# Performance work log

Measured on AMD Instinct MI355X. Metric: run time of the kernel, lower is better.

## Reference

```python
import jax, jax.numpy as jnp
import numpy as np

B, S, D_IN, D_OUT = 4, 2048, 1024, 1024

def setup_inputs() -> dict:
    key = jax.random.key(0)
    k1, k2, k3, k4, k5, k6 = jax.random.split(key, 6)
    return {
        "inputs_for_keys": jax.random.normal(k1, (B, S, D_IN), dtype=jnp.float32),
        "inputs_for_values": jax.random.normal(k2, (B, S, D_IN), dtype=jnp.float32),
        "inputs_for_queries": jax.random.normal(k3, (B, S, D_IN), dtype=jnp.float32),
        "WK": jax.random.truncated_normal(k4, -2.0, 2.0, (D_IN, D_OUT), dtype=jnp.float32) * 0.1,
        "WV": jax.random.truncated_normal(k5, -2.0, 2.0, (D_IN, D_OUT), dtype=jnp.float32) * 0.1,
        "WQ": jax.random.truncated_normal(k6, -2.0, 2.0, (D_IN, D_OUT), dtype=jnp.float32) * 0.1,
    }

def reference(inputs_for_keys, inputs_for_values, inputs_for_queries, WK, WV, WQ):
    # projections: [B,S,D_in] @ [D_in,D_out] -> [B,S,D_out]
    K = jnp.einsum('bsd,de->bse', inputs_for_keys, WK)
    V = jnp.einsum('bsd,de->bse', inputs_for_values, WV)
    Q = jnp.einsum('bsd,de->bse', inputs_for_queries, WQ)
    # scores: [B,S,S]. NOTE: original TF code scales by sqrt(K.shape[1]) = sqrt(seq_len),
    # not sqrt(head_dim) — reproduce that faithfully.
    scale = jnp.sqrt(jnp.float32(K.shape[1]))
    scores = jnp.einsum('bqe,bke->bqk', Q, K) / scale
    attn = jax.nn.softmax(scores, axis=-1)
    return jnp.einsum('bqk,bke->bqe', attn, V)
```

## Files before the change

kernel.cpp:

```cpp
#include <hip/hip_runtime.h>
#include <hip/hip_bf16.h>


typedef __attribute__((ext_vector_type(4))) float    f32x4;
typedef __attribute__((ext_vector_type(8))) _Float16 f16x8;
typedef __attribute__((ext_vector_type(4))) _Float16 f16x4;

constexpr size_t MiB = 1u << 20;
constexpr size_t MK  = (size_t)8192 * 1024;
constexpr size_t WSZ = (size_t)1024 * 1024;

__device__ __forceinline__ void gload_lds16(const void* g, void* l) {
  __builtin_amdgcn_global_load_lds(
      (const __attribute__((address_space(1))) unsigned int*)g,
      (__attribute__((address_space(3))) unsigned int*)l, 16, 0, 0);
}

#define MFMA16(a, b, c) __builtin_amdgcn_mfma_f32_16x16x32_f16(a, b, c, 0, 0, 0)

__device__ __forceinline__ void swz_block(int& bx, int& by, int& bz) {
  unsigned gx = gridDim.x, gy = gridDim.y;
  unsigned flat = blockIdx.x + gx * (blockIdx.y + gy * blockIdx.z);
  unsigned total = gx * gy * gridDim.z;
  unsigned cpx = total >> 3;
  unsigned s = (flat & 7) * cpx + (flat >> 3);
  bx = s % gx; s /= gx; by = s % gy; bz = s / gy;
}

__global__ __launch_bounds__(256) void convert_x(
    const float* __restrict__ x0, const float* __restrict__ x1,
    const float* __restrict__ x2, _Float16* __restrict__ XF)
{
  const int z = blockIdx.z;
  const float* x = z == 0 ? x0 : (z == 1 ? x1 : x2);
  size_t i = ((size_t)blockIdx.x * 256 + threadIdx.x) * 4;
  float4 v = *(const float4*)(x + i);
  f16x4 h = {(_Float16)v.x, (_Float16)v.y, (_Float16)v.z, (_Float16)v.w};
  *(f16x4*)(XF + (size_t)z * MK + i) = h;
}

__global__ __launch_bounds__(256) void transpose_conv_w(
    const float* __restrict__ w0, const float* __restrict__ w1,
    const float* __restrict__ w2, _Float16* __restrict__ WT)
{
  const int z = blockIdx.z;
  const float* W = z == 0 ? w0 : (z == 1 ? w1 : w2);
  _Float16* o = WT + (size_t)z * WSZ;
  __shared__ float tile[32][33];
  const int bx = blockIdx.x * 32;
  const int by = blockIdx.y * 32;
  const int tx = threadIdx.x & 31, ty = threadIdx.x >> 5;
  #pragma unroll
  for (int r = 0; r < 32; r += 8)
    tile[ty + r][tx] = W[(size_t)(by + ty + r) * 1024 + bx + tx];
  __syncthreads();
  #pragma unroll
  for (int r = 0; r < 32; r += 8)
    o[(size_t)(bx + ty + r) * 1024 + by + tx] = (_Float16)tile[tx][ty + r];
}

__global__ __launch_bounds__(256) void transpose_v(
    const _Float16* __restrict__ V, _Float16* __restrict__ Vt)
{
  const _Float16* v = V + (size_t)blockIdx.z * 2048 * 1024;
  _Float16* o = Vt + (size_t)blockIdx.z * 1024 * 2048;
  __shared__ _Float16 tile[32][33];
  const int bx = blockIdx.x * 32;
  const int by = blockIdx.y * 32;
  const int tx = threadIdx.x & 31, ty = threadIdx.x >> 5;
  #pragma unroll
  for (int r = 0; r < 32; r += 8)
    tile[ty + r][tx] = v[(size_t)(by + ty + r) * 1024 + bx + tx];
  __syncthreads();
  #pragma unroll
  for (int r = 0; r < 32; r += 8)
    o[(size_t)(bx + ty + r) * 2048 + by + tx] = tile[tx][ty + r];
}

template <int MODE>
__global__ __launch_bounds__(512, 2) void gemm256(
    const _Float16* __restrict__ At, size_t sA,
    const _Float16* __restrict__ Bt, size_t sB,
    void* __restrict__ C0v, size_t sCz,
    int N, int K, float scale)
{
  extern __shared__ char lds[];
  constexpr int BB = 128 * 64;
  char* ldsAb = lds;
  char* ldsBb = lds + 65536;

  int bx, by, bz;
  swz_block(bx, by, bz);
  const _Float16* A = At + (size_t)bz * sA;
  const _Float16* B = Bt + (size_t)bz * sB;

  const int gm0 = by * 256;
  const int gn0 = bx * 128;
  const int tid = threadIdx.x;
  const int lane = tid & 63, wave = tid >> 6;
  const int wm = (wave >> 1) * 64;
  const int wn = (wave & 1) * 64;
  const int fr = lane & 15, fq = lane >> 4;

  const int nkt = K >> 5;

  const int cbs = (((tid & 3) ^ ((tid >> 3) & 3)) << 4);
  const size_t aOff = (size_t)(gm0 + (tid >> 2)) * K + (cbs >> 1);
  const size_t bOff = (size_t)(gn0 + (tid >> 2)) * K + (cbs >> 1);
  const int cbr  = (fq * 16) ^ (((fr >> 1) & 3) << 4);
  const int arow = (wm + fr) * 64 + cbr;
  const int brow = (wn + fr) * 64 + cbr;

  f32x4 acc[4][4] = {};

  for (int tp = 0; tp < 3; ++tp) {
    const _Float16* gA = A + aOff + tp * 32;
    const _Float16* gB = B + bOff + tp * 32;
    char* dA = ldsAb + tp * 16384 + tid * 16;
    char* dB = ldsBb + tp * BB + tid * 16;
    gload_lds16(gA, dA);
    gload_lds16(gA + (size_t)128 * K, dA + 8192);
    gload_lds16(gB, dB);
  }
  asm volatile("s_waitcnt vmcnt(6)" ::: "memory");
  __builtin_amdgcn_s_barrier();
  __builtin_amdgcn_sched_barrier(0);

  for (int t = 0; t < nkt; ++t) {
    const char* pA = ldsAb + (t & 3) * 16384;
    const char* pB = ldsBb + (t & 3) * BB;
    const int tp = t + 3;
    const bool st = tp < nkt;
    const _Float16* gA = A + aOff + (st ? tp : 0) * 32;
    const _Float16* gB = B + bOff + (st ? tp : 0) * 32;
    char* dA = ldsAb + (tp & 3) * 16384 + tid * 16;
    char* dB = ldsBb + (tp & 3) * BB + tid * 16;

    if (st) { gload_lds16(gA, dA); gload_lds16(gB, dB); }
    f16x8 bfr[4], af[2];
    #pragma unroll
    for (int n = 0; n < 4; ++n) bfr[n] = *(const f16x8*)(pB + brow + n * 1024);
    #pragma unroll
    for (int m = 0; m < 2; ++m) af[m] = *(const f16x8*)(pA + arow + m * 1024);
    __builtin_amdgcn_s_setprio(1);
    #pragma unroll
    for (int m = 0; m < 2; ++m)
      #pragma unroll
      for (int n = 0; n < 4; ++n) acc[m][n] = MFMA16(af[m], bfr[n], acc[m][n]);
    __builtin_amdgcn_s_setprio(0);
    __builtin_amdgcn_s_barrier();
    __builtin_amdgcn_sched_barrier(0);

    if (st) gload_lds16(gA + (size_t)128 * K, dA + 8192);
    #pragma unroll
    for (int m = 0; m < 2; ++m) af[m] = *(const f16x8*)(pA + arow + (m + 2) * 1024);
    __builtin_amdgcn_s_setprio(1);
    #pragma unroll
    for (int m = 0; m < 2; ++m)
      #pragma unroll
      for (int n = 0; n < 4; ++n) acc[m + 2][n] = MFMA16(af[m], bfr[n], acc[m + 2][n]);
    __builtin_amdgcn_s_setprio(0);
    asm volatile("s_waitcnt vmcnt(6)" ::: "memory");
    __builtin_amdgcn_s_barrier();
    __builtin_amdgcn_sched_barrier(0);
  }

  const int erow = gm0 + wm + fq * 4;
  const int ecol = gn0 + wn + fr;
  if constexpr (MODE == 0) {
    float* C = (float*)C0v + (size_t)bz * sCz;
    #pragma unroll
    for (int m = 0; m < 4; ++m)
      #pragma unroll
      for (int n = 0; n < 4; ++n) {
        size_t base = (size_t)(erow + m * 16) * N + (ecol + n * 16);
        #pragma unroll
        for (int r = 0; r < 4; ++r)
          C[base + (size_t)r * N] = acc[m][n][r] * scale;
      }
  } else {
    _Float16* C = (_Float16*)C0v + (size_t)bz * sCz;
    #pragma unroll
    for (int m = 0; m < 4; ++m)
      #pragma unroll
      for (int n = 0; n < 4; ++n) {
        size_t base = (size_t)(erow + m * 16) * N + (ecol + n * 16);
        #pragma unroll
        for (int r = 0; r < 4; ++r)
          C[base + (size_t)r * N] = (_Float16)acc[m][n][r];
      }
  }
}

__global__ __launch_bounds__(256) void softmax_rows(
    const float* __restrict__ S, _Float16* __restrict__ P)
{
  const size_t row = blockIdx.x;
  const float4* srow = (const float4*)(S + row * 2048);
  const int t = threadIdx.x;
  float4 v0 = srow[t];
  float4 v1 = srow[t + 256];

  float m = fmaxf(fmaxf(fmaxf(v0.x, v0.y), fmaxf(v0.z, v0.w)),
                  fmaxf(fmaxf(v1.x, v1.y), fmaxf(v1.z, v1.w)));
  #pragma unroll
  for (int o = 32; o >= 1; o >>= 1) m = fmaxf(m, __shfl_xor(m, o));
  __shared__ float redm[4];
  if ((t & 63) == 0) redm[t >> 6] = m;
  __syncthreads();
  m = fmaxf(fmaxf(redm[0], redm[1]), fmaxf(redm[2], redm[3]));

  float e[8];
  e[0] = __expf(v0.x - m); e[1] = __expf(v0.y - m);
  e[2] = __expf(v0.z - m); e[3] = __expf(v0.w - m);
  e[4] = __expf(v1.x - m); e[5] = __expf(v1.y - m);
  e[6] = __expf(v1.z - m); e[7] = __expf(v1.w - m);
  float s = e[0] + e[1] + e[2] + e[3] + e[4] + e[5] + e[6] + e[7];
  #pragma unroll
  for (int o = 32; o >= 1; o >>= 1) s += __shfl_xor(s, o);
  __shared__ float reds[4];
  if ((t & 63) == 0) reds[t >> 6] = s;
  __syncthreads();
  s = reds[0] + reds[1] + reds[2] + reds[3];

  const float inv = 1.0f / s;
  f16x4 p0 = {(_Float16)(e[0] * inv), (_Float16)(e[1] * inv),
              (_Float16)(e[2] * inv), (_Float16)(e[3] * inv)};
  f16x4 p1 = {(_Float16)(e[4] * inv), (_Float16)(e[5] * inv),
              (_Float16)(e[6] * inv), (_Float16)(e[7] * inv)};
  f16x4* prow = (f16x4*)(P + row * 2048);
  prow[t] = p0;
  prow[t + 256] = p1;
}

extern "C" void kernel_launch(void* const* d_in, const int* in_sizes, int n_in,
                              void* d_out, int out_size, void* d_ws, size_t ws_size,
                              hipStream_t stream)
{
  const float* Xk = (const float*)d_in[0];
  const float* Xv = (const float*)d_in[1];
  const float* Xq = (const float*)d_in[2];
  const float* WK = (const float*)d_in[3];
  const float* WV = (const float*)d_in[4];
  const float* WQ = (const float*)d_in[5];
  float* out = (float*)d_out;
  char* ws = (char*)d_ws;

  _Float16* XF  = (_Float16*)(ws);
  _Float16* WT  = (_Float16*)(ws + 48 * MiB);
  _Float16* PROJ= (_Float16*)(ws + 54 * MiB);
  _Float16* VT  = (_Float16*)(ws + 102 * MiB);
  float*   SCORES = (float*)(ws + 118 * MiB);
  _Float16* P   = (_Float16*)(ws);

  _Float16* Kp = PROJ;
  _Float16* Vp = PROJ + MK;
  _Float16* Qp = PROJ + 2 * MK;

  auto* fP  = gemm256<1>;
  auto* fSC = gemm256<0>;
  (void)hipFuncSetAttribute((const void*)fP,  hipFuncAttributeMaxDynamicSharedMemorySize, 98304);
  (void)hipFuncSetAttribute((const void*)fSC, hipFuncAttributeMaxDynamicSharedMemorySize, 98304);

  convert_x<<<dim3(8192, 1, 3), 256, 0, stream>>>(Xk, Xv, Xq, XF);
  transpose_conv_w<<<dim3(32, 32, 3), 256, 0, stream>>>(WK, WV, WQ, WT);
  gemm256<1><<<dim3(8, 32, 3), 512, 98304, stream>>>(
      XF, MK, WT, WSZ, PROJ, MK, 1024, 1024, 1.0f);
  transpose_v<<<dim3(32, 64, 4), 256, 0, stream>>>(Vp, VT);
  gemm256<0><<<dim3(16, 8, 4), 512, 98304, stream>>>(
      Qp, (size_t)2048 * 1024, Kp, (size_t)2048 * 1024,
      SCORES, (size_t)2048 * 2048, 2048, 1024, 0.022097086912079608f);
  softmax_rows<<<dim3(8192), 256, 0, stream>>>(SCORES, P);
  gemm256<0><<<dim3(8, 8, 4), 512, 98304, stream>>>(
      P, (size_t)2048 * 2048, VT, (size_t)1024 * 2048,
      out, (size_t)2048 * 1024, 1024, 2048, 1.0f);
}
```

Measured before the change: 222.1 us.

## Add 256x256 eight-phase GEMM and store fp16 scores with wave-per-row softmax

Adds a new gemm8p kernel with 256x256 output tiles, 128 KiB double-buffered LDS and a four-phase interleaved load/MFMA schedule. It is used for the projection and QK^T GEMMs to raise data reuse per tile. The score matrix is now written in fp16 instead of fp32, which halves score traffic, and softmax is rewritten to one wave per row with no LDS reductions. Storing scaled scores in fp16 loses some precision, and the larger tiles mean fewer blocks, which lowers occupancy and load balance.

New measurement: 202.4 us. 1.1x faster.

```diff
diff --git a/kernel.cpp b/kernel.cpp
--- a/kernel.cpp
+++ b/kernel.cpp
@@ -75,6 +75,167 @@
   #pragma unroll
   for (int r = 0; r < 32; r += 8)
     o[(size_t)(bx + ty + r) * 2048 + by + tx] = tile[tx][ty + r];
+}
+
+template <int MODE>
+__global__ __launch_bounds__(512, 2) void gemm8p(
+    const _Float16* __restrict__ At, size_t sA,
+    const _Float16* __restrict__ Bt, size_t sB,
+    void* __restrict__ Cv, size_t sCz,
+    int N, int K, float scale)
+{
+  extern __shared__ char lds[];
+  int bx, by, bz;
+  swz_block(bx, by, bz);
+  const _Float16* A = At + (size_t)bz * sA;
+  const _Float16* B = Bt + (size_t)bz * sB;
+
+  const int gm0 = by * 256, gn0 = bx * 256;
+  const int tid = threadIdx.x;
+  const int lane = tid & 63, wave = tid >> 6;
+  const int wm = (wave >> 2) * 128;
+  const int wn = (wave & 3) * 64;
+  const int fr = lane & 15, fq = lane >> 4;
+  const int nkt = K >> 6;
+
+  const int clog = ((tid & 7) ^ ((tid >> 3) & 7)) * 8;
+  const _Float16* srcA = A + (size_t)(gm0 + (tid >> 3)) * K + clog;
+  const _Float16* srcB = B + (size_t)(gn0 + (tid >> 3)) * K + clog;
+  char* const dst0 = lds + tid * 16;
+
+  auto SH = [&](int tile, int h) {
+    const _Float16* s = (h < 2 ? srcA : srcB) + (size_t)((h & 1) * 128) * K
+                        + tile * 64;
+    char* d = dst0 + (tile & 1) * 65536 + h * 16384;
+    gload_lds16(s, d);
+    gload_lds16(s + (size_t)64 * K, d + 8192);
+  };
+
+  const int axor = fr & 7;
+  const int pc0 = (fq ^ axor) * 16;
+  const int pc1 = ((4 + fq) ^ axor) * 16;
+  const int arb = (wm + fr) * 128;
+  const int brb = 32768 + (wn + fr) * 128;
+
+  f32x4 acc[8][4] = {};
+  f16x8 af[4][2], b0[2][2], b1[2][2];
+
+  SH(0, 0); SH(0, 1); SH(0, 2); SH(0, 3);
+  if (nkt > 1) {
+    SH(1, 0);
+    asm volatile("s_waitcnt vmcnt(2)" ::: "memory");
+  } else {
+    asm volatile("s_waitcnt vmcnt(0)" ::: "memory");
+  }
+  __builtin_amdgcn_s_barrier();
+  __builtin_amdgcn_sched_barrier(0);
+
+#define PHASE_MID                                          \
+  __builtin_amdgcn_s_barrier();                            \
+  asm volatile("s_waitcnt lgkmcnt(0)" ::: "memory");       \
+  __builtin_amdgcn_sched_barrier(0);                       \
+  __builtin_amdgcn_s_setprio(1);
+#define PHASE_END                                          \
+  __builtin_amdgcn_s_setprio(0);                           \
+  __builtin_amdgcn_sched_barrier(0);                       \
+  __builtin_amdgcn_s_barrier();
+
+  for (int t = 0; t < nkt; ++t) {
+    const char* buf = lds + (t & 1) * 65536;
+    const bool st1 = (t + 1) < nkt;
+
+    #pragma unroll
+    for (int mi = 0; mi < 4; ++mi) {
+      af[mi][0] = *(const f16x8*)(buf + arb + mi * 2048 + pc0);
+      af[mi][1] = *(const f16x8*)(buf + arb + mi * 2048 + pc1);
+    }
+    #pragma unroll
+    for (int ni = 0; ni < 2; ++ni) {
+      b0[ni][0] = *(const f16x8*)(buf + brb + ni * 2048 + pc0);
+      b0[ni][1] = *(const f16x8*)(buf + brb + ni * 2048 + pc1);
+    }
+    if (st1) SH(t + 1, 1);
+    PHASE_MID
+    #pragma unroll
+    for (int mi = 0; mi < 4; ++mi)
+      #pragma unroll
+      for (int ni = 0; ni < 2; ++ni)
+        #pragma unroll
+        for (int kk = 0; kk < 2; ++kk)
+          acc[mi][ni] = MFMA16(af[mi][kk], b0[ni][kk], acc[mi][ni]);
+    PHASE_END
+
+    #pragma unroll
+    for (int ni = 0; ni < 2; ++ni) {
+      b1[ni][0] = *(const f16x8*)(buf + brb + (ni + 2) * 2048 + pc0);
+      b1[ni][1] = *(const f16x8*)(buf + brb + (ni + 2) * 2048 + pc1);
+    }
+    if (st1) SH(t + 1, 2);
+    PHASE_MID
+    #pragma unroll
+    for (int mi = 0; mi < 4; ++mi)
+      #pragma unroll
+      for (int ni = 0; ni < 2; ++ni)
+        #pragma unroll
+        for (int kk = 0; kk < 2; ++kk)
+          acc[mi][ni + 2] = MFMA16(af[mi][kk], b1[ni][kk], acc[mi][ni + 2]);
+    PHASE_END
+
+    #pragma unroll
+    for (int mi = 0; mi < 4; ++mi) {
+      af[mi][0] = *(const f16x8*)(buf + arb + (mi + 4) * 2048 + pc0);
+      af[mi][1] = *(const f16x8*)(buf + arb + (mi + 4) * 2048 + pc1);
+    }
+    if (st1) SH(t + 1, 3);
+    PHASE_MID
+    #pragma unroll
+    for (int mi = 0; mi < 4; ++mi)
+      #pragma unroll
+      for (int ni = 0; ni < 2; ++ni)
+        #pragma unroll
+        for (int kk = 0; kk < 2; ++kk)
+          acc[mi + 4][ni] = MFMA16(af[mi][kk], b0[ni][kk], acc[mi + 4][ni]);
+    PHASE_END
+
+    const bool st2 = (t + 2) < nkt;
+    if (st2) SH(t + 2, 0);
+    __builtin_amdgcn_s_barrier();
+    __builtin_amdgcn_s_setprio(1);
+    #pragma unroll
+    for (int mi = 0; mi < 4; ++mi)
+      #pragma unroll
+      for (int ni = 0; ni < 2; ++ni)
+        #pragma unroll
+        for (int kk = 0; kk < 2; ++kk)
+          acc[mi + 4][ni + 2] = MFMA16(af[mi][kk], b1[ni][kk], acc[mi + 4][ni + 2]);
+    __builtin_amdgcn_s_setprio(0);
+    __builtin_amdgcn_sched_barrier(0);
+    if (st2) asm volatile("s_waitcnt vmcnt(2)" ::: "memory");
+    else     asm volatile("s_waitcnt vmcnt(0)" ::: "memory");
+    __builtin_amdgcn_s_barrier();
+  }
+#undef PHASE_MID
+#undef PHASE_END
+
+  const int erow = gm0 + wm + fq * 4;
+  const int ecol = gn0 + wn + fr;
+  #pragma unroll
+  for (int m = 0; m < 8; ++m)
+    #pragma unroll
+    for (int n = 0; n < 4; ++n) {
+      size_t base = (size_t)(erow + m * 16) * N + (ecol + n * 16);
+      #pragma unroll
+      for (int r = 0; r < 4; ++r) {
+        float v = acc[m][n][r];
+        if constexpr (MODE == 0)
+          ((float*)Cv + (size_t)bz * sCz)[base + (size_t)r * N] = v * scale;
+        else if constexpr (MODE == 1)
+          ((_Float16*)Cv + (size_t)bz * sCz)[base + (size_t)r * N] = (_Float16)v;
+        else
+          ((_Float16*)Cv + (size_t)bz * sCz)[base + (size_t)r * N] =
+              (_Float16)(v * scale);
+      }
+    }
 }
 
 template <int MODE>
@@ -167,70 +328,59 @@
 
   const int erow = gm0 + wm + fq * 4;
   const int ecol = gn0 + wn + fr;
-  if constexpr (MODE == 0) {
-    float* C = (float*)C0v + (size_t)bz * sCz;
-    #pragma unroll
-    for (int m = 0; m < 4; ++m)
-      #pragma unroll
-      for (int n = 0; n < 4; ++n) {
-        size_t base = (size_t)(erow + m * 16) * N + (ecol + n * 16);
-        #pragma unroll
-        for (int r = 0; r < 4; ++r)
-          C[base + (size_t)r * N] = acc[m][n][r] * scale;
-      }
-  } else {
-    _Float16* C = (_Float16*)C0v + (size_t)bz * sCz;
-    #pragma unroll
-    for (int m = 0; m < 4; ++m)
-      #pragma unroll
-      for (int n = 0; n < 4; ++n) {
-        size_t base = (size_t)(erow + m * 16) * N + (ecol + n * 16);
-        #pragma unroll
-        for (int r = 0; r < 4; ++r)
-          C[base + (size_t)r * N] = (_Float16)acc[m][n][r];
-      }
+  float* C = (float*)C0v + (size_t)bz * sCz;
+  #pragma unroll
+  for (int m = 0; m < 4; ++m)
+    #pragma unroll
+    for (int n = 0; n < 4; ++n) {
+      size_t base = (size_t)(erow + m * 16) * N + (ecol + n * 16);
+      #pragma unroll
+      for (int r = 0; r < 4; ++r)
+        C[base + (size_t)r * N] = acc[m][n][r] * scale;
+    }
+}
+
+__global__ __launch_bounds__(256) void softmax_rows(
+    const _Float16* __restrict__ S, _Float16* __restrict__ P)
+{
+  const int w = threadIdx.x >> 6, lane = threadIdx.x & 63;
+  const size_t row = (size_t)blockIdx.x * 4 + w;
+  const _Float16* sr = S + row * 2048;
+
+  f16x8 v[4];
+  #pragma unroll
+  for (int c = 0; c < 4; ++c)
+    v[c] = *(const f16x8*)(sr + c * 512 + lane * 8);
+
+  float m = -1e30f;
+  #pragma unroll
+  for (int c = 0; c < 4; ++c)
+    #pragma unroll
+    for (int j = 0; j < 8; ++j) m = fmaxf(m, (float)v[c][j]);
+  #pragma unroll
+  for (int o = 32; o >= 1; o >>= 1) m = fmaxf(m, __shfl_xor(m, o));
+
+  float e[4][8];
+  float s = 0.f;
+  #pragma unroll
+  for (int c = 0; c < 4; ++c)
+    #pragma unroll
+    for (int j = 0; j < 8; ++j) {
+      e[c][j] = __expf((float)v[c][j] - m);
+      s += e[c][j];
+    }
+  #pragma unroll
+  for (int o = 32; o >= 1; o >>= 1) s += __shfl_xor(s, o);
+
+  const float inv = 1.0f / s;
+  _Float16* pr = P + row * 2048;
+  #pragma unroll
+  for (int c = 0; c < 4; ++c) {
+    f16x8 p;
+    #pragma unroll
+    for (int j = 0; j < 8; ++j) p[j] = (_Float16)(e[c][j] * inv);
+    *(f16x8*)(pr + c * 512 + lane * 8) = p;
   }
-}
-
-__global__ __launch_bounds__(256) void softmax_rows(
-    const float* __restrict__ S, _Float16* __restrict__ P)
-{
-  const size_t row = blockIdx.x;
-  const float4* srow = (const float4*)(S + row * 2048);
-  const int t = threadIdx.x;
-  float4 v0 = srow[t];
-  float4 v1 = srow[t + 256];
-
-  float m = fmaxf(fmaxf(fmaxf(v0.x, v0.y), fmaxf(v0.z, v0.w)),
-                  fmaxf(fmaxf(v1.x, v1.y), fmaxf(v1.z, v1.w)));
-  #pragma unroll
-  for (int o = 32; o >= 1; o >>= 1) m = fmaxf(m, __shfl_xor(m, o));
-  __shared__ float redm[4];
-  if ((t & 63) == 0) redm[t >> 6] = m;
-  __syncthreads();
-  m = fmaxf(fmaxf(redm[0], redm[1]), fmaxf(redm[2], redm[3]));
-
-  float e[8];
-  e[0] = __expf(v0.x - m); e[1] = __expf(v0.y - m);
-  e[2] = __expf(v0.z - m); e[3] = __expf(v0.w - m);
-  e[4] = __expf(v1.x - m); e[5] = __expf(v1.y - m);
-  e[6] = __expf(v1.z - m); e[7] = __expf(v1.w - m);
-  float s = e[0] + e[1] + e[2] + e[3] + e[4] + e[5] + e[6] + e[7];
-  #pragma unroll
-  for (int o = 32; o >= 1; o >>= 1) s += __shfl_xor(s, o);
-  __shared__ float reds[4];
-  if ((t & 63) == 0) reds[t >> 6] = s;
-  __syncthreads();
-  s = reds[0] + reds[1] + reds[2] + reds[3];
-
-  const float inv = 1.0f / s;
-  f16x4 p0 = {(_Float16)(e[0] * inv), (_Float16)(e[1] * inv),
-              (_Float16)(e[2] * inv), (_Float16)(e[3] * inv)};
-  f16x4 p1 = {(_Float16)(e[4] * inv), (_Float16)(e[5] * inv),
-              (_Float16)(e[6] * inv), (_Float16)(e[7] * inv)};
-  f16x4* prow = (f16x4*)(P + row * 2048);
-  prow[t] = p0;
-  prow[t + 256] = p1;
 }
 
 extern "C" void kernel_launch(void* const* d_in, const int* in_sizes, int n_in,
@@ -246,31 +396,33 @@
   float* out = (float*)d_out;
   char* ws = (char*)d_ws;
 
-  _Float16* XF  = (_Float16*)(ws);
-  _Float16* WT  = (_Float16*)(ws + 48 * MiB);
-  _Float16* PROJ= (_Float16*)(ws + 54 * MiB);
-  _Float16* VT  = (_Float16*)(ws + 102 * MiB);
-  float*   SCORES = (float*)(ws + 118 * MiB);
-  _Float16* P   = (_Float16*)(ws);
+  _Float16* XF   = (_Float16*)(ws);
+  _Float16* WT   = (_Float16*)(ws + 48 * MiB);
+  _Float16* PROJ = (_Float16*)(ws + 54 * MiB);
+  _Float16* VT   = (_Float16*)(ws + 102 * MiB);
+  _Float16* SC   = (_Float16*)(ws + 118 * MiB);
+  _Float16* P    = (_Float16*)(ws);
 
   _Float16* Kp = PROJ;
   _Float16* Vp = PROJ + MK;
   _Float16* Qp = PROJ + 2 * MK;
 
-  auto* fP  = gemm256<1>;
-  auto* fSC = gemm256<0>;
-  (void)hipFuncSetAttribute((const void*)fP,  hipFuncAttributeMaxDynamicSharedMemorySize, 98304);
-  (void)hipFuncSetAttribute((const void*)fSC, hipFuncAttributeMaxDynamicSharedMemorySize, 98304);
+  auto* fP  = gemm8p<1>;
+  auto* fSC = gemm8p<2>;
+  auto* fPV = gemm256<0>;
+  (void)hipFuncSetAttribute((const void*)fP,  hipFuncAttributeMaxDynamicSharedMemorySize, 131072);
+  (void)hipFuncSetAttribute((const void*)fSC, hipFuncAttributeMaxDynamicSharedMemorySize, 131072);
+  (void)hipFuncSetAttribute((const void*)fPV, hipFuncAttributeMaxDynamicSharedMemorySize, 98304);
 
   convert_x<<<dim3(8192, 1, 3), 256, 0, stream>>>(Xk, Xv, Xq, XF);
   transpose_conv_w<<<dim3(32, 32, 3), 256, 0, stream>>>(WK, WV, WQ, WT);
-  gemm256<1><<<dim3(8, 32, 3), 512, 98304, stream>>>(
+  gemm8p<1><<<dim3(4, 32, 3), 512, 131072, stream>>>(
       XF, MK, WT, WSZ, PROJ, MK, 1024, 1024, 1.0f);
   transpose_v<<<dim3(32, 64, 4), 256, 0, stream>>>(Vp, VT);
-  gemm256<0><<<dim3(16, 8, 4), 512, 98304, stream>>>(
+  gemm8p<2><<<dim3(8, 8, 4), 512, 131072, stream>>>(
       Qp, (size_t)2048 * 1024, Kp, (size_t)2048 * 1024,
-      SCORES, (size_t)2048 * 2048, 2048, 1024, 0.022097086912079608f);
-  softmax_rows<<<dim3(8192), 256, 0, stream>>>(SCORES, P);
+      SC, (size_t)2048 * 2048, 2048, 1024, 0.022097086912079608f);
+  softmax_rows<<<dim3(2048), 256, 0, stream>>>(SC, P);
   gemm256<0><<<dim3(8, 8, 4), 512, 98304, stream>>>(
       P, (size_t)2048 * 2048, VT, (size_t)1024 * 2048,
       out, (size_t)2048 * 1024, 1024, 2048, 1.0f);
```

## Rework GEMM pipeline to 3-stage buffers, store scores in fp16, wave-per-row softmax

Applied to the files above, without the earlier changes.

The GEMM kernel drops from a 4-deep split-phase LDS pipeline (96KB) to a 3-deep single-phase pipeline (72KB) with one barrier per k-tile, a new swizzle pattern and a higher occupancy hint in launch bounds. The attention scores are now written in fp16 rather than fp32, which halves score write and read traffic. Softmax processes one row per wave using shuffle reductions only, with no LDS reductions or block syncs. The fp16 scores lose some precision before the softmax, and the shallower prefetch may hide less memory latency.

Measured after the change: 208.1 us. 1.07x faster.

```diff
diff --git a/kernel.cpp b/kernel.cpp
--- a/kernel.cpp
+++ b/kernel.cpp
@@ -78,159 +78,145 @@
 }
 
 template <int MODE>
-__global__ __launch_bounds__(512, 2) void gemm256(
+__global__ __launch_bounds__(512, 4) void gemmO(
     const _Float16* __restrict__ At, size_t sA,
     const _Float16* __restrict__ Bt, size_t sB,
-    void* __restrict__ C0v, size_t sCz,
+    void* __restrict__ Cv, size_t sCz,
     int N, int K, float scale)
 {
   extern __shared__ char lds[];
-  constexpr int BB = 128 * 64;
-  char* ldsAb = lds;
-  char* ldsBb = lds + 65536;
-
   int bx, by, bz;
   swz_block(bx, by, bz);
   const _Float16* A = At + (size_t)bz * sA;
   const _Float16* B = Bt + (size_t)bz * sB;
 
-  const int gm0 = by * 256;
-  const int gn0 = bx * 128;
+  const int gm0 = by * 256, gn0 = bx * 128;
   const int tid = threadIdx.x;
   const int lane = tid & 63, wave = tid >> 6;
   const int wm = (wave >> 1) * 64;
   const int wn = (wave & 1) * 64;
   const int fr = lane & 15, fq = lane >> 4;
-
   const int nkt = K >> 5;
 
-  const int cbs = (((tid & 3) ^ ((tid >> 3) & 3)) << 4);
-  const size_t aOff = (size_t)(gm0 + (tid >> 2)) * K + (cbs >> 1);
-  const size_t bOff = (size_t)(gn0 + (tid >> 2)) * K + (cbs >> 1);
-  const int cbr  = (fq * 16) ^ (((fr >> 1) & 3) << 4);
-  const int arow = (wm + fr) * 64 + cbr;
-  const int brow = (wn + fr) * 64 + cbr;
+  const int clog = ((tid & 3) ^ ((tid >> 2) & 3)) * 8;
+  const _Float16* srcA = A + (size_t)(gm0 + (tid >> 2)) * K + clog;
+  const _Float16* srcB = B + (size_t)(gn0 + (tid >> 2)) * K + clog;
+  char* const dst0 = lds + tid * 16;
+
+  auto STG = [&](int tile) {
+    const int off = tile * 32;
+    char* d = dst0 + (tile % 3) * 24576;
+    gload_lds16(srcA + off,                  d);
+    gload_lds16(srcA + off + (size_t)128 * K, d + 8192);
+    gload_lds16(srcB + off,                  d + 16384);
+  };
+
+  const int pc  = (fq ^ (fr & 3)) * 16;
+  const int arb = (wm + fr) * 64 + pc;
+  const int brb = 16384 + (wn + fr) * 64 + pc;
 
   f32x4 acc[4][4] = {};
-
-  for (int tp = 0; tp < 3; ++tp) {
-    const _Float16* gA = A + aOff + tp * 32;
-    const _Float16* gB = B + bOff + tp * 32;
-    char* dA = ldsAb + tp * 16384 + tid * 16;
-    char* dB = ldsBb + tp * BB + tid * 16;
-    gload_lds16(gA, dA);
-    gload_lds16(gA + (size_t)128 * K, dA + 8192);
-    gload_lds16(gB, dB);
+  f16x8 af[4], bfr[4];
+
+  STG(0);
+  if (nkt > 1) {
+    STG(1);
+    asm volatile("s_waitcnt vmcnt(3)" ::: "memory");
+  } else {
+    asm volatile("s_waitcnt vmcnt(0)" ::: "memory");
   }
-  asm volatile("s_waitcnt vmcnt(6)" ::: "memory");
   __builtin_amdgcn_s_barrier();
   __builtin_amdgcn_sched_barrier(0);
 
   for (int t = 0; t < nkt; ++t) {
-    const char* pA = ldsAb + (t & 3) * 16384;
-    const char* pB = ldsBb + (t & 3) * BB;
-    const int tp = t + 3;
-    const bool st = tp < nkt;
-    const _Float16* gA = A + aOff + (st ? tp : 0) * 32;
-    const _Float16* gB = B + bOff + (st ? tp : 0) * 32;
-    char* dA = ldsAb + (tp & 3) * 16384 + tid * 16;
-    char* dB = ldsBb + (tp & 3) * BB + tid * 16;
-
-    if (st) { gload_lds16(gA, dA); gload_lds16(gB, dB); }
-    f16x8 bfr[4], af[2];
-    #pragma unroll
-    for (int n = 0; n < 4; ++n) bfr[n] = *(const f16x8*)(pB + brow + n * 1024);
-    #pragma unroll
-    for (int m = 0; m < 2; ++m) af[m] = *(const f16x8*)(pA + arow + m * 1024);
+    const char* buf = lds + (t % 3) * 24576;
+    const bool st2 = (t + 2) < nkt;
+
+    if (st2) STG(t + 2);
+
+    #pragma unroll
+    for (int mi = 0; mi < 4; ++mi)
+      af[mi] = *(const f16x8*)(buf + arb + mi * 1024);
+    #pragma unroll
+    for (int ni = 0; ni < 4; ++ni)
+      bfr[ni] = *(const f16x8*)(buf + brb + ni * 1024);
+
     __builtin_amdgcn_s_setprio(1);
     #pragma unroll
-    for (int m = 0; m < 2; ++m)
+    for (int mi = 0; mi < 4; ++mi)
       #pragma unroll
-      for (int n = 0; n < 4; ++n) acc[m][n] = MFMA16(af[m], bfr[n], acc[m][n]);
+      for (int ni = 0; ni < 4; ++ni)
+        acc[mi][ni] = MFMA16(af[mi], bfr[ni], acc[mi][ni]);
     __builtin_amdgcn_s_setprio(0);
-    __builtin_amdgcn_s_barrier();
-    __builtin_amdgcn_sched_barrier(0);
-
-    if (st) gload_lds16(gA + (size_t)128 * K, dA + 8192);
-    #pragma unroll
-    for (int m = 0; m < 2; ++m) af[m] = *(const f16x8*)(pA + arow + (m + 2) * 1024);
-    __builtin_amdgcn_s_setprio(1);
-    #pragma unroll
-    for (int m = 0; m < 2; ++m)
-      #pragma unroll
-      for (int n = 0; n < 4; ++n) acc[m + 2][n] = MFMA16(af[m], bfr[n], acc[m + 2][n]);
-    __builtin_amdgcn_s_setprio(0);
-    asm volatile("s_waitcnt vmcnt(6)" ::: "memory");
+
+    if (st2)               asm volatile("s_waitcnt vmcnt(3)" ::: "memory");
+    else if (t + 1 < nkt)  asm volatile("s_waitcnt vmcnt(0)" ::: "memory");
     __builtin_amdgcn_s_barrier();
     __builtin_amdgcn_sched_barrier(0);
   }
 
   const int erow = gm0 + wm + fq * 4;
   const int ecol = gn0 + wn + fr;
-  if constexpr (MODE == 0) {
-    float* C = (float*)C0v + (size_t)bz * sCz;
-    #pragma unroll
-    for (int m = 0; m < 4; ++m)
+  #pragma unroll
+  for (int m = 0; m < 4; ++m)
+    #pragma unroll
+    for (int n = 0; n < 4; ++n) {
+      size_t base = (size_t)(erow + m * 16) * N + (ecol + n * 16);
       #pragma unroll
-      for (int n = 0; n < 4; ++n) {
-        size_t base = (size_t)(erow + m * 16) * N + (ecol + n * 16);
-        #pragma unroll
-        for (int r = 0; r < 4; ++r)
-          C[base + (size_t)r * N] = acc[m][n][r] * scale;
+      for (int r = 0; r < 4; ++r) {
+        float v = acc[m][n][r];
+        if constexpr (MODE == 0)
+          ((float*)Cv + (size_t)bz * sCz)[base + (size_t)r * N] = v * scale;
+        else if constexpr (MODE == 1)
+          ((_Float16*)Cv + (size_t)bz * sCz)[base + (size_t)r * N] = (_Float16)v;
+        else
+          ((_Float16*)Cv + (size_t)bz * sCz)[base + (size_t)r * N] =
+              (_Float16)(v * scale);
       }
-  } else {
-    _Float16* C = (_Float16*)C0v + (size_t)bz * sCz;
-    #pragma unroll
-    for (int m = 0; m < 4; ++m)
-      #pragma unroll
-      for (int n = 0; n < 4; ++n) {
-        size_t base = (size_t)(erow + m * 16) * N + (ecol + n * 16);
-        #pragma unroll
-        for (int r = 0; r < 4; ++r)
-          C[base + (size_t)r * N] = (_Float16)acc[m][n][r];
-      }
+    }
+}
+
+__global__ __launch_bounds__(256) void softmax_rows(
+    const _Float16* __restrict__ S, _Float16* __restrict__ P)
+{
+  const int w = threadIdx.x >> 6, lane = threadIdx.x & 63;
+  const size_t row = (size_t)blockIdx.x * 4 + w;
+  const _Float16* sr = S + row * 2048;
+
+  f16x8 v[4];
+  #pragma unroll
+  for (int c = 0; c < 4; ++c)
+    v[c] = *(const f16x8*)(sr + c * 512 + lane * 8);
+
+  float m = -1e30f;
+  #pragma unroll
+  for (int c = 0; c < 4; ++c)
+    #pragma unroll
+    for (int j = 0; j < 8; ++j) m = fmaxf(m, (float)v[c][j]);
+  #pragma unroll
+  for (int o = 32; o >= 1; o >>= 1) m = fmaxf(m, __shfl_xor(m, o));
+
+  float e[4][8];
+  float s = 0.f;
+  #pragma unroll
+  for (int c = 0; c < 4; ++c)
+    #pragma unroll
+    for (int j = 0; j < 8; ++j) {
+      e[c][j] = __expf((float)v[c][j] - m);
+      s += e[c][j];
+    }
+  #pragma unroll
+  for (int o = 32; o >= 1; o >>= 1) s += __shfl_xor(s, o);
+
+  const float inv = 1.0f / s;
+  _Float16* pr = P + row * 2048;
+  #pragma unroll
+  for (int c = 0; c < 4; ++c) {
+    f16x8 p;
+    #pragma unroll
+    for (int j = 0; j < 8; ++j) p[j] = (_Float16)(e[c][j] * inv);
+    *(f16x8*)(pr + c * 512 + lane * 8) = p;
   }
-}
-
-__global__ __launch_bounds__(256) void softmax_rows(
-    const float* __restrict__ S, _Float16* __restrict__ P)
-{
-  const size_t row = blockIdx.x;
-  const float4* srow = (const float4*)(S + row * 2048);
-  const int t = threadIdx.x;
-  float4 v0 = srow[t];
-  float4 v1 = srow[t + 256];
-
-  float m = fmaxf(fmaxf(fmaxf(v0.x, v0.y), fmaxf(v0.z, v0.w)),
-                  fmaxf(fmaxf(v1.x, v1.y), fmaxf(v1.z, v1.w)));
-  #pragma unroll
-  for (int o = 32; o >= 1; o >>= 1) m = fmaxf(m, __shfl_xor(m, o));
-  __shared__ float redm[4];
-  if ((t & 63) == 0) redm[t >> 6] = m;
-  __syncthreads();
-  m = fmaxf(fmaxf(redm[0], redm[1]), fmaxf(redm[2], redm[3]));
-
-  float e[8];
-  e[0] = __expf(v0.x - m); e[1] = __expf(v0.y - m);
-  e[2] = __expf(v0.z - m); e[3] = __expf(v0.w - m);
-  e[4] = __expf(v1.x - m); e[5] = __expf(v1.y - m);
-  e[6] = __expf(v1.z - m); e[7] = __expf(v1.w - m);
-  float s = e[0] + e[1] + e[2] + e[3] + e[4] + e[5] + e[6] + e[7];
-  #pragma unroll
-  for (int o = 32; o >= 1; o >>= 1) s += __shfl_xor(s, o);
-  __shared__ float reds[4];
-  if ((t & 63) == 0) reds[t >> 6] = s;
-  __syncthreads();
-  s = reds[0] + reds[1] + reds[2] + reds[3];
-
-  const float inv = 1.0f / s;
-  f16x4 p0 = {(_Float16)(e[0] * inv), (_Float16)(e[1] * inv),
-              (_Float16)(e[2] * inv), (_Float16)(e[3] * inv)};
-  f16x4 p1 = {(_Float16)(e[4] * inv), (_Float16)(e[5] * inv),
-              (_Float16)(e[6] * inv), (_Float16)(e[7] * inv)};
-  f16x4* prow = (f16x4*)(P + row * 2048);
-  prow[t] = p0;
-  prow[t + 256] = p1;
 }
 
 extern "C" void kernel_launch(void* const* d_in, const int* in_sizes, int n_in,
@@ -246,32 +232,34 @@
   float* out = (float*)d_out;
   char* ws = (char*)d_ws;
 
-  _Float16* XF  = (_Float16*)(ws);
-  _Float16* WT  = (_Float16*)(ws + 48 * MiB);
-  _Float16* PROJ= (_Float16*)(ws + 54 * MiB);
-  _Float16* VT  = (_Float16*)(ws + 102 * MiB);
-  float*   SCORES = (float*)(ws + 118 * MiB);
-  _Float16* P   = (_Float16*)(ws);
+  _Float16* XF   = (_Float16*)(ws);
+  _Float16* WT   = (_Float16*)(ws + 48 * MiB);
+  _Float16* PROJ = (_Float16*)(ws + 54 * MiB);
+  _Float16* VT   = (_Float16*)(ws + 102 * MiB);
+  _Float16* SC   = (_Float16*)(ws + 118 * MiB);
+  _Float16* P    = (_Float16*)(ws);
 
   _Float16* Kp = PROJ;
   _Float16* Vp = PROJ + MK;
   _Float16* Qp = PROJ + 2 * MK;
 
-  auto* fP  = gemm256<1>;
-  auto* fSC = gemm256<0>;
-  (void)hipFuncSetAttribute((const void*)fP,  hipFuncAttributeMaxDynamicSharedMemorySize, 98304);
-  (void)hipFuncSetAttribute((const void*)fSC, hipFuncAttributeMaxDynamicSharedMemorySize, 98304);
+  auto* fP  = gemmO<1>;
+  auto* fSC = gemmO<2>;
+  auto* fPV = gemmO<0>;
+  (void)hipFuncSetAttribute((const void*)fP,  hipFuncAttributeMaxDynamicSharedMemorySize, 73728);
+  (void)hipFuncSetAttribute((const void*)fSC, hipFuncAttributeMaxDynamicSharedMemorySize, 73728);
+  (void)hipFuncSetAttribute((const void*)fPV, hipFuncAttributeMaxDynamicSharedMemorySize, 73728);
 
   convert_x<<<dim3(8192, 1, 3), 256, 0, stream>>>(Xk, Xv, Xq, XF);
   transpose_conv_w<<<dim3(32, 32, 3), 256, 0, stream>>>(WK, WV, WQ, WT);
-  gemm256<1><<<dim3(8, 32, 3), 512, 98304, stream>>>(
+  gemmO<1><<<dim3(8, 32, 3), 512, 73728, stream>>>(
       XF, MK, WT, WSZ, PROJ, MK, 1024, 1024, 1.0f);
   transpose_v<<<dim3(32, 64, 4), 256, 0, stream>>>(Vp, VT);
-  gemm256<0><<<dim3(16, 8, 4), 512, 98304, stream>>>(
+  gemmO<2><<<dim3(16, 8, 4), 512, 73728, stream>>>(
       Qp, (size_t)2048 * 1024, Kp, (size_t)2048 * 1024,
-      SCORES, (size_t)2048 * 2048, 2048, 1024, 0.022097086912079608f);
-  softmax_rows<<<dim3(8192), 256, 0, stream>>>(SCORES, P);
-  gemm256<0><<<dim3(8, 8, 4), 512, 98304, stream>>>(
+      SC, (size_t)2048 * 2048, 2048, 1024, 0.022097086912079608f);
+  softmax_rows<<<dim3(2048), 256, 0, stream>>>(SC, P);
+  gemmO<0><<<dim3(8, 8, 4), 512, 73728, stream>>>(
       P, (size_t)2048 * 2048, VT, (size_t)1024 * 2048,
       out, (size_t)2048 * 1024, 1024, 2048, 1.0f);
 }
```
